# Optimization experiments

Measured on AMD Instinct MI355X. Metric: run time of the kernel, lower is better.

The kernel has to match this reference:

```python
import jax, jax.numpy as jnp
import numpy as np

NH = 12  # attention heads (bert-base)


def _ln(x, s, b, eps=1e-12):
    mu = x.mean(-1, keepdims=True)
    var = ((x - mu) ** 2).mean(-1, keepdims=True)
    return (x - mu) / jnp.sqrt(var + eps) * s + b


def _forward(input_ids, token_type_ids, attention_mask, word_emb, pos_emb, type_emb,
             emb_ln_s, emb_ln_b, memory, q_w, q_b, k_w, k_b, v_w, v_b, o_w, o_b,
             ln1_s, ln1_b, f_w1, f_b1, f_w2, f_b2, ln2_s, ln2_b,
             key_w1, key_b1, key_w2, key_b2, val_w1, val_b1, val_w2, val_b2):
    B, S = input_ids.shape
    M, H = memory.shape
    T = S + M
    m = attention_mask.astype(jnp.int32)          # [B,S] 0/1
    L = m.sum(-1)                                 # [B] number of real tokens
    tok_emb = word_emb[input_ids]                 # [B,S,H]
    # stable argsort puts mask==1 positions first (in original order), then mask==0
    order = jnp.argsort(1 - m, axis=-1)           # [B,S]
    p = jnp.arange(T)[None, :]                    # [1,T]
    Lb = L[:, None]
    # output layout per sample: [real tokens (L), memory (M), pad tokens (S-L)]
    src_p = jnp.clip(jnp.where(p < Lb, p, p - M), 0, S - 1)
    src_idx = jnp.take_along_axis(order, src_p, axis=1)                  # [B,T]
    gathered = jnp.take_along_axis(tok_emb, src_idx[..., None], axis=1)  # [B,T,H]
    is_mem = (p >= Lb) & (p < Lb + M)
    mem_idx = jnp.clip(p - Lb, 0, M - 1)
    emb = jnp.where(is_mem[..., None], memory[mem_idx], gathered)        # spliced embeds
    att = (p < Lb + M).astype(emb.dtype)                                 # [B,T]
    tt = jnp.where(p < Lb, jnp.take_along_axis(token_type_ids.astype(jnp.int32), src_idx, axis=1), 1)
    # --- BERT encoder on inputs_embeds ---
    x = _ln(emb + pos_emb[None, :T] + type_emb[tt], emb_ln_s, emb_ln_b)
    bias = ((1.0 - att) * -10000.0)[:, None, None, :]                    # [B,1,1,T]
    dh = H // NH
    for l in range(q_w.shape[0]):
        q = (x @ q_w[l] + q_b[l]).reshape(B, T, NH, dh)
        k = (x @ k_w[l] + k_b[l]).reshape(B, T, NH, dh)
        v = (x @ v_w[l] + v_b[l]).reshape(B, T, NH, dh)
        s = jnp.einsum('bqhd,bkhd->bhqk', q, k) / jnp.sqrt(jnp.asarray(dh, x.dtype)) + bias
        a = jax.nn.softmax(s, axis=-1)
        ctx = jnp.einsum('bhqk,bkhd->bqhd', a, v).reshape(B, T, H)
        x = _ln(x + ctx @ o_w[l] + o_b[l], ln1_s[l], ln1_b[l])
        h = jax.nn.gelu(x @ f_w1[l] + f_b1[l], approximate=False)
        x = _ln(x + h @ f_w2[l] + f_b2[l], ln2_s[l], ln2_b[l])
    # --- gated key/value softmax pooling (get_rep_no_vae) ---
    value = jnp.tanh(jax.nn.relu(x @ val_w1 + val_b1) @ val_w2 + val_b2)       # [B,T,E]
    weight = jax.nn.sigmoid(jax.nn.relu(x @ key_w1 + key_b1) @ key_w2 + key_b2)  # [B,T,E]
    pool_mask = jnp.where(tt == 1, -jnp.inf, 0.0).astype(x.dtype)[..., None]   # [B,T,1]
    fw = jax.nn.softmax(weight + pool_mask, axis=-2)  # softmax over token dim
    return jax.nn.relu((fw * value).sum(-2))          # [B,E]


def setup_inputs() -> dict:
    key = jax.random.key(0)
    ks = jax.random.split(key, 20)
    B, S, M, H, E, V, NL, FF = 8, 512, 64, 768, 512, 30522, 2, 3072
    def rn(k, shape, s=0.02):
        return jax.random.normal(k, shape, jnp.float32) * s
    return {
        'input_ids': jax.random.randint(ks[0], (B, S), 0, V),
        'token_type_ids': jnp.zeros((B, S), jnp.int32),
        'attention_mask': jax.random.randint(ks[1], (B, S), 0, 2),
        'word_emb': rn(ks[2], (V, H)),
        'pos_emb': rn(ks[3], (S + M, H)),
        'type_emb': rn(ks[4], (2, H)),
        'emb_ln_s': jnp.ones((H,), jnp.float32), 'emb_ln_b': jnp.zeros((H,), jnp.float32),
        'memory': rn(ks[5], (M, H), 1.0),
        'q_w': rn(ks[6], (NL, H, H)), 'q_b': jnp.zeros((NL, H), jnp.float32),
        'k_w': rn(ks[7], (NL, H, H)), 'k_b': jnp.zeros((NL, H), jnp.float32),
        'v_w': rn(ks[8], (NL, H, H)), 'v_b': jnp.zeros((NL, H), jnp.float32),
        'o_w': rn(ks[9], (NL, H, H)), 'o_b': jnp.zeros((NL, H), jnp.float32),
        'ln1_s': jnp.ones((NL, H), jnp.float32), 'ln1_b': jnp.zeros((NL, H), jnp.float32),
        'f_w1': rn(ks[10], (NL, H, FF)), 'f_b1': jnp.zeros((NL, FF), jnp.float32),
        'f_w2': rn(ks[11], (NL, FF, H)), 'f_b2': jnp.zeros((NL, H), jnp.float32),
        'ln2_s': jnp.ones((NL, H), jnp.float32), 'ln2_b': jnp.zeros((NL, H), jnp.float32),
        'key_w1': rn(ks[12], (H, 2 * H)), 'key_b1': jnp.zeros((2 * H,), jnp.float32),
        'key_w2': rn(ks[13], (2 * H, E)), 'key_b2': jnp.zeros((E,), jnp.float32),
        'val_w1': rn(ks[14], (H, 2 * E)), 'val_b1': jnp.zeros((2 * E,), jnp.float32),
        'val_w2': rn(ks[15], (2 * E, E)), 'val_b2': jnp.zeros((E,), jnp.float32),
    }


def reference(input_ids, token_type_ids, attention_mask, word_emb, pos_emb, type_emb,
              emb_ln_s, emb_ln_b, memory, q_w, q_b, k_w, k_b, v_w, v_b, o_w, o_b,
              ln1_s, ln1_b, f_w1, f_b1, f_w2, f_b2, ln2_s, ln2_b,
              key_w1, key_b1, key_w2, key_b2, val_w1, val_b1, val_w2, val_b2):
    return _forward(input_ids, token_type_ids, attention_mask, word_emb, pos_emb, type_emb,
                    emb_ln_s, emb_ln_b, memory, q_w, q_b, k_w, k_b, v_w, v_b, o_w, o_b,
                    ln1_s, ln1_b, f_w1, f_b1, f_w2, f_b2, ln2_s, ln2_b,
                    key_w1, key_b1, key_w2, key_b2, val_w1, val_b1, val_w2, val_b2)
```

## Files before the change

kernel.cpp:

```cpp
#include <hip/hip_runtime.h>
#include <hip/hip_bf16.h>

#define B 8
#define S 512
#define MM 64
#define T 576
#define H 768
#define NH 12
#define DH 64
#define FF 3072
#define E 512
#define NL 2

typedef __attribute__((ext_vector_type(8))) short bf16x8;
typedef __attribute__((ext_vector_type(4))) float f32x4;

__device__ inline unsigned short bf16_rne(float f) {
    unsigned u = __builtin_bit_cast(unsigned, f);
    unsigned r = u + 0x7FFFu + ((u >> 16) & 1u);
    return (unsigned short)(r >> 16);
}

__device__ inline f32x4 mfma16(bf16x8 a, bf16x8 b, f32x4 c) {
    return __builtin_amdgcn_mfma_f32_16x16x32_bf16(a, b, c, 0, 0, 0);
}

__device__ inline void load_lds16(const void* g, void* l) {
    __builtin_amdgcn_global_load_lds((const __attribute__((address_space(1))) void*)g,
                                     (__attribute__((address_space(3))) void*)l, 16, 0, 0);
}

__global__ void embed_kernel(const int* __restrict__ ids, const int* __restrict__ toktype,
                             const int* __restrict__ ord, const int* __restrict__ Larr,
                             int* __restrict__ boff, int* __restrict__ rowb,
                             const float* __restrict__ word_emb, const float* __restrict__ pos_emb,
                             const float* __restrict__ type_emb, const float* __restrict__ memory,
                             const float* __restrict__ lns, const float* __restrict__ lnb,
                             float* __restrict__ x, unsigned short* __restrict__ xb,
                             int* __restrict__ ttarr) {
    int t = blockIdx.x;
    int b = blockIdx.y;
    int pre[B + 1];
    {
        int acc = 0;
        #pragma unroll
        for (int b2 = 0; b2 < B; ++b2) { pre[b2] = acc; acc += Larr[b2] + MM; }
        pre[B] = acc;
    }
    int Lb = Larr[b];
    int tid = threadIdx.x;
    if (t == 0 && b == 0) {
        if (tid <= B) boff[tid] = pre[tid];
        for (int r = tid; r < B * T; r += 256) {
            int bb = 0;
            #pragma unroll
            for (int b2 = 1; b2 < B; ++b2) bb += (r >= pre[b2]) ? 1 : 0;
            rowb[r] = bb;
        }
    }
    if (t >= Lb + MM) return;
    int row = pre[b] + t;
    int tt;
    const float* src;
    if (t < Lb) {
        int sp = ord[b * S + t];
        tt = toktype[b * S + sp];
        src = &word_emb[(size_t)ids[b * S + sp] * H];
    } else {
        tt = 1;
        src = &memory[(size_t)(t - Lb) * H];
    }
    __shared__ float rowv[H];
    __shared__ float r1[256], r2[256];
    float lsum = 0.f, lsq = 0.f;
    for (int hh = tid; hh < H; hh += 256) {
        float v = src[hh] + pos_emb[(size_t)t * H + hh] + type_emb[(size_t)tt * H + hh];
        rowv[hh] = v;
        lsum += v;
        lsq += v * v;
    }
    r1[tid] = lsum; r2[tid] = lsq;
    __syncthreads();
    for (int s = 128; s > 0; s >>= 1) {
        if (tid < s) { r1[tid] += r1[tid + s]; r2[tid] += r2[tid + s]; }
        __syncthreads();
    }
    float mu = r1[0] / H;
    float var = r2[0] / H - mu * mu;
    float inv = rsqrtf(var + 1e-12f);
    for (int hh = tid; hh < H; hh += 256) {
        float v = (rowv[hh] - mu) * inv * lns[hh] + lnb[hh];
        x[(size_t)row * H + hh] = v;
        xb[(size_t)row * H + hh] = bf16_rne(v);
    }
    if (tid == 0) ttarr[row] = tt;
}

#define ACT_NONE 0
#define ACT_RELU 1
#define ACT_GELU 2
#define ACT_SIGMOID 3
#define ACT_TANH 4

template <int ACT>
__device__ inline float apply_act(float v) {
    if constexpr (ACT == ACT_RELU) return fmaxf(v, 0.f);
    else if constexpr (ACT == ACT_GELU) {
        float y = v * 0.70710678118654752f;
        float a = fabsf(y);
        float t = 1.f / (1.f + 0.3275911f * a);
        float poly = t * (0.254829592f + t * (-0.284496736f + t * (1.421413741f +
                     t * (-1.453152027f + t * 1.061405429f))));
        float e = poly * exp2f(-a * a * 1.4426950408889634f);
        float erfv = 1.f - e;
        erfv = (y < 0.f) ? -erfv : erfv;
        return 0.5f * v * (1.f + erfv);
    }
    else if constexpr (ACT == ACT_SIGMOID) return 1.f / (1.f + expf(-v));
    else if constexpr (ACT == ACT_TANH) return tanhf(v);
    else return v;
}

#define NT_TILES 17024
struct TDesc { const float* src; unsigned dstoff; int Kd; int Nd; int tile0; };
struct TTab { TDesc d[16]; int n; };

__global__ __launch_bounds__(256) void transpose_all(TTab tab, unsigned short* __restrict__ dstbase,
                                                     const int* __restrict__ mask,
                                                     int* __restrict__ ord, int* __restrict__ Larr) {
    int tile = blockIdx.x;
    int tid = threadIdx.x;
    if (tile >= NT_TILES) {
        int b = tile - NT_TILES;
        __shared__ int ps[S];
        int m0 = (mask[b * S + tid] != 0) ? 1 : 0;
        int m1 = (mask[b * S + tid + 256] != 0) ? 1 : 0;
        ps[tid] = m0; ps[tid + 256] = m1;
        __syncthreads();
        for (int off2 = 1; off2 < S; off2 <<= 1) {
            int a0 = (tid >= off2) ? ps[tid - off2] : 0;
            int a1 = (tid + 256 >= off2) ? ps[tid + 256 - off2] : 0;
            __syncthreads();
            ps[tid] += a0; ps[tid + 256] += a1;
            __syncthreads();
        }
        int L = ps[S - 1];
        int r0 = m0 ? (ps[tid] - 1) : (L + (tid - ps[tid]));
        int r1 = m1 ? (ps[tid + 256] - 1) : (L + (tid + 256 - ps[tid + 256]));
        ord[b * S + r0] = tid;
        ord[b * S + r1] = tid + 256;
        if (tid == 0) Larr[b] = L;
        return;
    }
    int mi = 0;
    #pragma unroll
    for (int i = 1; i < 16; ++i)
        if (i < tab.n && tab.d[i].tile0 <= tile) mi = i;
    TDesc d = tab.d[mi];
    int rel = tile - d.tile0;
    int tilesK = d.Kd >> 5;
    int kt = rel % tilesK, nt = rel / tilesK;
    __shared__ float ts[32][33];
    int k0 = kt * 32, n0 = nt * 32;
    int tx = tid & 31, ty = tid >> 5;
    #pragma unroll
    for (int r = 0; r < 4; ++r) {
        int kk = ty + r * 8;
        ts[kk][tx] = d.src[(size_t)(k0 + kk) * d.Nd + n0 + tx];
    }
    __syncthreads();
    unsigned short* Wt = dstbase + d.dstoff;
    #pragma unroll
    for (int r = 0; r < 4; ++r) {
        int nn = ty + r * 8;
        Wt[(size_t)(n0 + nn) * d.Kd + k0 + tx] = bf16_rne(ts[tx][nn]);
    }
}

#define EPI_F32   0
#define EPI_BF16  1
#define EPI_QKV   2
#define EPI_SPLIT2 3

template <int ACT, int EPI, int NSPLIT>
__global__ __launch_bounds__(256) void mfma_gemm(
    const unsigned short* __restrict__ A, const unsigned short* __restrict__ Bt,
    const float* __restrict__ b0, const float* __restrict__ b1, const float* __restrict__ b2,
    int sp1, int sp2,
    float* __restrict__ Cf, float* __restrict__ Cf2,
    float* __restrict__ Cf3, float* __restrict__ Cf4,
    unsigned short* __restrict__ Cb, unsigned short* __restrict__ Cb2,
    unsigned short* __restrict__ Vt, int n2w,
    const int* __restrict__ boffs, const int* __restrict__ rowb,
    int Mdim, int Ndim, int Kdim) {
    __shared__ unsigned short As[3][128 * 32];
    __shared__ unsigned short Bs[3][128 * 32];

    const int bn = blockIdx.x * 128, bm = blockIdx.y * 128;

    const int Mtot = boffs[B];
    if (bm >= Mtot) return;

    const int z = (NSPLIT > 1) ? blockIdx.z : 0;
    const int Klocal = Kdim / NSPLIT;
    const int koff = z * Klocal;

    const int tid = threadIdx.x;
    const int w = tid >> 6, lane = tid & 63;
    const int lr = lane & 15, g = lane >> 4;
    const int wr = w >> 1, wc = w & 1;
    f32x4 acc[4][4] = {};

    const int srow = w * 32 + (lane >> 2);
    const int kc = (((lane & 3) ^ ((lane >> 4) & 3)) * 8);
    const unsigned short* ga0 = A + (size_t)(bm + srow) * Kdim + kc;
    const unsigned short* ga1 = A + (size_t)(bm + srow + 16) * Kdim + kc;
    const unsigned short* gb0 = Bt + (size_t)(bn + srow) * Kdim + kc;
    const unsigned short* gb1 = Bt + (size_t)(bn + srow + 16) * Kdim + kc;
    const int d0 = (w * 32) * 32, d1 = (w * 32 + 16) * 32;

    const int sw = ((g ^ ((lr >> 2) & 3)) & 3) * 8;

    auto stage = [&](int pp, int k0) {
        load_lds16(ga0 + k0, &As[pp][d0]);
        load_lds16(ga1 + k0, &As[pp][d1]);
        load_lds16(gb0 + k0, &Bs[pp][d0]);
        load_lds16(gb1 + k0, &Bs[pp][d1]);
    };
    auto compute = [&](int pp) {
        bf16x8 af[4], bfr[4];
        #pragma unroll
        for (int i = 0; i < 4; ++i)
            af[i] = *(const bf16x8*)&As[pp][(wr * 64 + i * 16 + lr) * 32 + sw];
        #pragma unroll
        for (int j = 0; j < 4; ++j)
            bfr[j] = *(const bf16x8*)&Bs[pp][(wc * 64 + j * 16 + lr) * 32 + sw];
        __builtin_amdgcn_s_setprio(1);
        #pragma unroll
        for (int i = 0; i < 4; ++i)
            #pragma unroll
            for (int j = 0; j < 4; ++j)
                acc[i][j] = mfma16(af[i], bfr[j], acc[i][j]);
        __builtin_amdgcn_s_setprio(0);
    };

    const int nk = Klocal >> 5;
    stage(0, koff);
    int p = 0;
    for (int s = 0; s < nk; ++s) {
        if (s + 1 < nk) {
            int pn = p + 1; if (pn == 3) pn = 0;
            stage(pn, koff + (s + 1) * 32);
            asm volatile("s_waitcnt vmcnt(4)" ::: "memory");
        } else {
            asm volatile("s_waitcnt vmcnt(0)" ::: "memory");
        }
        __builtin_amdgcn_s_barrier();
        __builtin_amdgcn_sched_barrier(0);
        compute(p);
        __builtin_amdgcn_sched_barrier(0);
        p = (p == 2) ? 0 : p + 1;
    }

    float* Cdst = (z == 0) ? Cf : (z == 1) ? Cf2 : (z == 2) ? Cf3 : Cf4;
    #pragma unroll
    for (int i = 0; i < 4; ++i) {
        const int row0 = bm + wr * 64 + i * 16 + 4 * g;
        #pragma unroll
        for (int j = 0; j < 4; ++j) {
            const int col = bn + wc * 64 + j * 16 + lr;
            float bv = (NSPLIT > 1 && z != 0) ? 0.f
                     : ((col < sp1) ? b0[col] : (col < sp2 ? b1[col - sp1] : b2[col - sp2]));
            float vv[4];
            #pragma unroll
            for (int r = 0; r < 4; ++r) vv[r] = apply_act<ACT>(acc[i][j][r] + bv);
            if constexpr (EPI == EPI_F32) {
                #pragma unroll
                for (int r = 0; r < 4; ++r) Cdst[(size_t)(row0 + r) * Ndim + col] = vv[r];
            } else if constexpr (EPI == EPI_BF16) {
                #pragma unroll
                for (int r = 0; r < 4; ++r) Cb[(size_t)(row0 + r) * Ndim + col] = bf16_rne(vv[r]);
            } else if constexpr (EPI == EPI_QKV) {
                if (col < 1536) {
                    #pragma unroll
                    for (int r = 0; r < 4; ++r) Cb[(size_t)(row0 + r) * 1536 + col] = bf16_rne(vv[r]);
                } else {
                    int c2 = col - 1536;
                    int hh2 = c2 >> 6, dd = c2 & 63;
                    int bb = rowb[row0];
                    if (row0 + 3 < Mtot && rowb[row0 + 3] == bb) {
                        int t0 = row0 - boffs[bb];
                        unsigned lo = (unsigned)bf16_rne(vv[0]) | ((unsigned)bf16_rne(vv[1]) << 16);
                        unsigned hi = (unsigned)bf16_rne(vv[2]) | ((unsigned)bf16_rne(vv[3]) << 16);
                        size_t idxv = (((size_t)bb * NH + hh2) * DH + dd) * T + t0;
                        *(uint2*)&Vt[idxv] = make_uint2(lo, hi);
                    } else {
                        #pragma unroll
                        for (int r = 0; r < 4; ++r) {
                            int rr = row0 + r;
                            if (rr < Mtot) {
                                int b2 = rowb[rr];
                                int t2 = rr - boffs[b2];
                                Vt[(((size_t)b2 * NH + hh2) * DH + dd) * T + t2] = bf16_rne(vv[r]);
                            }
                        }
                    }
                }
            } else {
                if (col < sp1) {
                    #pragma unroll
                    for (int r = 0; r < 4; ++r) Cb[(size_t)(row0 + r) * sp1 + col] = bf16_rne(vv[r]);
                } else {
                    #pragma unroll
                    for (int r = 0; r < 4; ++r)
                        Cb2[(size_t)(row0 + r) * n2w + (col - sp1)] = bf16_rne(vv[r]);
                }
            }
        }
    }
}

__global__ __launch_bounds__(256) void head2_gemm(
    const unsigned short* __restrict__ Ak, const unsigned short* __restrict__ Btk,
    const float* __restrict__ biask,
    const unsigned short* __restrict__ Av, const unsigned short* __restrict__ Btv,
    const float* __restrict__ biasv,
    float* __restrict__ P0, float* __restrict__ P1, float* __restrict__ P2, float* __restrict__ P3,
    float* __restrict__ V0, float* __restrict__ V1, float* __restrict__ V2, float* __restrict__ V3,
    const int* __restrict__ boffs) {
    __shared__ unsigned short As[3][128 * 32];
    __shared__ unsigned short Bs[3][128 * 32];

    const int bn = blockIdx.x * 128, bm = blockIdx.y * 128;
    const int Mtot = boffs[B];
    if (bm >= Mtot) return;

    const int z = blockIdx.z;
    const int isval = z >> 2, zk = z & 3;
    const unsigned short* A  = isval ? Av : Ak;
    const unsigned short* Bt = isval ? Btv : Btk;
    const float* bias = isval ? biasv : biask;
    const int Kdim = isval ? 1024 : 1536;
    const int Klocal = Kdim >> 2;
    const int koff = zk * Klocal;
    float* Cdst = isval ? ((zk == 0) ? V0 : (zk == 1) ? V1 : (zk == 2) ? V2 : V3)
                        : ((zk == 0) ? P0 : (zk == 1) ? P1 : (zk == 2) ? P2 : P3);

    const int tid = threadIdx.x;
    const int w = tid >> 6, lane = tid & 63;
    const int lr = lane & 15, g = lane >> 4;
    const int wr = w >> 1, wc = w & 1;
    f32x4 acc[4][4] = {};

    const int srow = w * 32 + (lane >> 2);
    const int kc = (((lane & 3) ^ ((lane >> 4) & 3)) * 8);
    const unsigned short* ga0 = A + (size_t)(bm + srow) * Kdim + kc;
    const unsigned short* ga1 = A + (size_t)(bm + srow + 16) * Kdim + kc;
    const unsigned short* gb0 = Bt + (size_t)(bn + srow) * Kdim + kc;
    const unsigned short* gb1 = Bt + (size_t)(bn + srow + 16) * Kdim + kc;
    const int d0 = (w * 32) * 32, d1 = (w * 32 + 16) * 32;
    const int sw = ((g ^ ((lr >> 2) & 3)) & 3) * 8;

    auto stage = [&](int pp, int k0) {
        load_lds16(ga0 + k0, &As[pp][d0]);
        load_lds16(ga1 + k0, &As[pp][d1]);
        load_lds16(gb0 + k0, &Bs[pp][d0]);
        load_lds16(gb1 + k0, &Bs[pp][d1]);
    };
    auto compute = [&](int pp) {
        bf16x8 af[4], bfr[4];
        #pragma unroll
        for (int i = 0; i < 4; ++i)
            af[i] = *(const bf16x8*)&As[pp][(wr * 64 + i * 16 + lr) * 32 + sw];
        #pragma unroll
        for (int j = 0; j < 4; ++j)
            bfr[j] = *(const bf16x8*)&Bs[pp][(wc * 64 + j * 16 + lr) * 32 + sw];
        __builtin_amdgcn_s_setprio(1);
        #pragma unroll
        for (int i = 0; i < 4; ++i)
            #pragma unroll
            for (int j = 0; j < 4; ++j)
                acc[i][j] = mfma16(af[i], bfr[j], acc[i][j]);
        __builtin_amdgcn_s_setprio(0);
    };

    const int nk = Klocal >> 5;
    stage(0, koff);
    int p = 0;
    for (int s = 0; s < nk; ++s) {
        if (s + 1 < nk) {
            int pn = p + 1; if (pn == 3) pn = 0;
            stage(pn, koff + (s + 1) * 32);
            asm volatile("s_waitcnt vmcnt(4)" ::: "memory");
        } else {
            asm volatile("s_waitcnt vmcnt(0)" ::: "memory");
        }
        __builtin_amdgcn_s_barrier();
        __builtin_amdgcn_sched_barrier(0);
        compute(p);
        __builtin_amdgcn_sched_barrier(0);
        p = (p == 2) ? 0 : p + 1;
    }

    #pragma unroll
    for (int i = 0; i < 4; ++i) {
        const int row0 = bm + wr * 64 + i * 16 + 4 * g;
        #pragma unroll
        for (int j = 0; j < 4; ++j) {
            const int col = bn + wc * 64 + j * 16 + lr;
            float bv = (zk == 0) ? bias[col] : 0.f;
            #pragma unroll
            for (int r = 0; r < 4; ++r)
                Cdst[(size_t)(row0 + r) * E + col] = acc[i][j][r] + bv;
        }
    }
}

#define C2 0.180336880111116670f
#define MB2 14426.950408889634f

__global__ __launch_bounds__(256) void attn_mfma(
    const unsigned short* __restrict__ QK, const unsigned short* __restrict__ Vt,
    const int* __restrict__ Larr, const int* __restrict__ boffs,
    unsigned short* __restrict__ ctxb) {
    const int n = blockIdx.x;
    const int xcd = n & 7, k = n >> 3;
    const int p = xcd * 12 + k / 9, qt = k % 9;
    const int b = p / NH, h = p % NH;
    const int LbMM = Larr[b] + MM;
    if (qt * 64 >= LbMM) return;
    const int w = threadIdx.x >> 6, lane = threadIdx.x & 63;
    const int q0 = qt * 64 + w * 16;
    if (q0 >= LbMM) return;
    const int base = boffs[b];
    const int lr = lane & 15, g = lane >> 4;
    __shared__ unsigned short P[4][16][72];
    const unsigned short* qrow = QK + (size_t)(base + q0 + lr) * 1536 + h * 64;
    bf16x8 qf0 = *(const bf16x8*)(qrow + 8 * g);
    bf16x8 qf1 = *(const bf16x8*)(qrow + 32 + 8 * g);
    f32x4 ctx[4] = {};
    float m_run = -1e30f, l_run = 0.f;
    const size_t vbase = ((size_t)b * NH + h) * DH;
    for (int kt = 0; kt < LbMM; kt += 64) {
        f32x4 sf[4];
        #pragma unroll
        for (int i = 0; i < 4; ++i) {
            const unsigned short* krow =
                QK + (size_t)(base + kt + 16 * i + lr) * 1536 + 768 + h * 64;
            bf16x8 kf0 = *(const bf16x8*)(krow + 8 * g);
            bf16x8 kf1 = *(const bf16x8*)(krow + 32 + 8 * g);
            f32x4 s = {};
            s = mfma16(kf0, qf0, s);
            s = mfma16(kf1, qf1, s);
            sf[i] = s;
        }
        float tmax = -1e30f;
        #pragma unroll
        for (int i = 0; i < 4; ++i)
            #pragma unroll
            for (int r = 0; r < 4; ++r) {
                int key = kt + 16 * i + 4 * g + r;
                float v = sf[i][r] * C2 + (key < LbMM ? 0.f : -MB2);
                sf[i][r] = v;
                tmax = fmaxf(tmax, v);
            }
        tmax = fmaxf(tmax, __shfl_xor(tmax, 16));
        tmax = fmaxf(tmax, __shfl_xor(tmax, 32));
        float m_new = fmaxf(m_run, tmax);
        float scale = exp2f(m_run - m_new);
        m_run = m_new;
        float psum = 0.f;
        #pragma unroll
        for (int i = 0; i < 4; ++i)
            #pragma unroll
            for (int r = 0; r < 4; ++r) {
                float pv = exp2f(sf[i][r] - m_new);
                sf[i][r] = pv;
                psum += pv;
            }
        l_run = l_run * scale + psum;
        float f0 = __shfl(scale, 4 * g + 0);
        float f1 = __shfl(scale, 4 * g + 1);
        float f2 = __shfl(scale, 4 * g + 2);
        float f3 = __shfl(scale, 4 * g + 3);
        #pragma unroll
        for (int j = 0; j < 4; ++j) {
            ctx[j][0] *= f0; ctx[j][1] *= f1; ctx[j][2] *= f2; ctx[j][3] *= f3;
        }
        #pragma unroll
        for (int i = 0; i < 4; ++i) {
            unsigned lo = (unsigned)bf16_rne(sf[i][0]) | ((unsigned)bf16_rne(sf[i][1]) << 16);
            unsigned hi = (unsigned)bf16_rne(sf[i][2]) | ((unsigned)bf16_rne(sf[i][3]) << 16);
            *(unsigned*)&P[w][lr][16 * i + 4 * g] = lo;
            *(unsigned*)&P[w][lr][16 * i + 4 * g + 2] = hi;
        }
        asm volatile("s_waitcnt lgkmcnt(0)" ::: "memory");
        __builtin_amdgcn_sched_barrier(0);
        #pragma unroll
        for (int s2 = 0; s2 < 2; ++s2) {
            bf16x8 pa = *(const bf16x8*)&P[w][lr][32 * s2 + 8 * g];
            #pragma unroll
            for (int j = 0; j < 4; ++j) {
                const unsigned short* vrow =
                    Vt + (vbase + 16 * j + lr) * T + kt + 32 * s2 + 8 * g;
                bf16x8 vf = *(const bf16x8*)vrow;
                ctx[j] = mfma16(pa, vf, ctx[j]);
            }
        }
        asm volatile("s_waitcnt lgkmcnt(0)" ::: "memory");
        __builtin_amdgcn_sched_barrier(0);
    }
    l_run += __shfl_xor(l_run, 16);
    l_run += __shfl_xor(l_run, 32);
    float inv = 1.f / l_run;
    float i0 = __shfl(inv, 4 * g + 0);
    float i1 = __shfl(inv, 4 * g + 1);
    float i2 = __shfl(inv, 4 * g + 2);
    float i3 = __shfl(inv, 4 * g + 3);
    float sc[4] = {i0, i1, i2, i3};
    #pragma unroll
    for (int j = 0; j < 4; ++j)
        #pragma unroll
        for (int r = 0; r < 4; ++r) {
            int rl = q0 + 4 * g + r;
            if (rl < LbMM)
                ctxb[(size_t)(base + rl) * H + h * 64 + 16 * j + lr] =
                    bf16_rne(ctx[j][r] * sc[r]);
        }
}

__global__ void lnres_kernel(float* __restrict__ x, const float* __restrict__ d1,
                             const float* __restrict__ d2, const float* __restrict__ d3,
                             const float* __restrict__ d4,
                             const float* __restrict__ s, const float* __restrict__ bvec,
                             unsigned short* __restrict__ xb, const int* __restrict__ mtotp) {
    int r = blockIdx.x;
    if (r >= mtotp[0]) return;
    int tid = threadIdx.x;
    __shared__ float4 row[H / 4];
    __shared__ float r1[256], r2[256];
    float lsum = 0.f, lsq = 0.f;
    size_t off4 = (size_t)r * (H / 4);
    if (tid < H / 4) {
        float4 a = ((const float4*)x)[off4 + tid];
        float4 p1 = ((const float4*)d1)[off4 + tid];
        float4 p2 = ((const float4*)d2)[off4 + tid];
        float4 p3 = ((const float4*)d3)[off4 + tid];
        float4 p4 = ((const float4*)d4)[off4 + tid];
        float4 v = make_float4(a.x + p1.x + p2.x + p3.x + p4.x,
                               a.y + p1.y + p2.y + p3.y + p4.y,
                               a.z + p1.z + p2.z + p3.z + p4.z,
                               a.w + p1.w + p2.w + p3.w + p4.w);
        row[tid] = v;
        lsum = v.x + v.y + v.z + v.w;
        lsq = v.x * v.x + v.y * v.y + v.z * v.z + v.w * v.w;
    }
    r1[tid] = lsum; r2[tid] = lsq;
    __syncthreads();
    for (int ss = 128; ss > 0; ss >>= 1) {
        if (tid < ss) { r1[tid] += r1[tid + ss]; r2[tid] += r2[tid + ss]; }
        __syncthreads();
    }
    float mu = r1[0] / H;
    float var = r2[0] / H - mu * mu;
    float inv = rsqrtf(var + 1e-12f);
    if (tid < H / 4) {
        float4 v = row[tid];
        const float4 sv = ((const float4*)s)[tid];
        const float4 bv = ((const float4*)bvec)[tid];
        float4 o = make_float4((v.x - mu) * inv * sv.x + bv.x,
                               (v.y - mu) * inv * sv.y + bv.y,
                               (v.z - mu) * inv * sv.z + bv.z,
                               (v.w - mu) * inv * sv.w + bv.w);
        ((float4*)x)[off4 + tid] = o;
        ushort4 ob = make_ushort4(bf16_rne(o.x), bf16_rne(o.y), bf16_rne(o.z), bf16_rne(o.w));
        *(ushort4*)&xb[(size_t)r * H + tid * 4] = ob;
    }
}

__global__ __launch_bounds__(256) void pool_kernel(
    const float* __restrict__ w0, const float* __restrict__ w1,
    const float* __restrict__ w2, const float* __restrict__ w3,
    const float* __restrict__ v0, const float* __restrict__ v1,
    const float* __restrict__ v2, const float* __restrict__ v3,
    const int* __restrict__ ttarr, const int* __restrict__ boffs,
    float* __restrict__ out) {
    int b = blockIdx.x;
    int le = threadIdx.x & 31;
    int e = blockIdx.y * 32 + le;
    int tg = threadIdx.x >> 5;
    int base = boffs[b];
    int nrow = boffs[b + 1] - base;
    __shared__ int ttl[T];
    __shared__ float red[8][33];
    for (int t = threadIdx.x; t < nrow; t += 256) ttl[t] = ttarr[base + t];
    __syncthreads();
    float mx = -1e30f;
    for (int t = tg; t < nrow; t += 8) {
        if (ttl[t] == 1) continue;
        size_t idx = (size_t)(base + t) * E + e;
        float w = 1.f / (1.f + expf(-(w0[idx] + w1[idx] + w2[idx] + w3[idx])));
        mx = fmaxf(mx, w);
    }
    red[tg][le] = mx;
    __syncthreads();
    #pragma unroll
    for (int i = 0; i < 8; ++i) mx = fmaxf(mx, red[i][le]);
    float den = 0.f, num = 0.f;
    for (int t = tg; t < nrow; t += 8) {
        if (ttl[t] == 1) continue;
        size_t idx = (size_t)(base + t) * E + e;
        float w = 1.f / (1.f + expf(-(w0[idx] + w1[idx] + w2[idx] + w3[idx])));
        float vval = tanhf(v0[idx] + v1[idx] + v2[idx] + v3[idx]);
        float ew = expf(w - mx);
        den += ew;
        num = fmaf(ew, vval, num);
    }
    __syncthreads();
    red[tg][le] = den;
    __syncthreads();
    float dtot = 0.f;
    #pragma unroll
    for (int i = 0; i < 8; ++i) dtot += red[i][le];
    __syncthreads();
    red[tg][le] = num;
    __syncthreads();
    float ntot = 0.f;
    #pragma unroll
    for (int i = 0; i < 8; ++i) ntot += red[i][le];
    if (tg == 0) out[(size_t)b * E + e] = fmaxf(ntot / dtot, 0.f);
}

extern "C" void kernel_launch(void* const* d_in, const int* in_sizes, int n_in,
                              void* d_out, int out_size, void* d_ws, size_t ws_size,
                              hipStream_t stream) {
    const int*   input_ids  = (const int*)d_in[0];
    const int*   token_type = (const int*)d_in[1];
    const int*   attn_mask  = (const int*)d_in[2];
    const float* word_emb   = (const float*)d_in[3];
    const float* pos_emb    = (const float*)d_in[4];
    const float* type_emb   = (const float*)d_in[5];
    const float* emb_ln_s   = (const float*)d_in[6];
    const float* emb_ln_b   = (const float*)d_in[7];
    const float* memory     = (const float*)d_in[8];
    const float* q_w  = (const float*)d_in[9];
    const float* q_b  = (const float*)d_in[10];
    const float* k_w  = (const float*)d_in[11];
    const float* k_b  = (const float*)d_in[12];
    const float* v_w  = (const float*)d_in[13];
    const float* v_b  = (const float*)d_in[14];
    const float* o_w  = (const float*)d_in[15];
    const float* o_b  = (const float*)d_in[16];
    const float* ln1_s = (const float*)d_in[17];
    const float* ln1_b = (const float*)d_in[18];
    const float* f_w1  = (const float*)d_in[19];
    const float* f_b1  = (const float*)d_in[20];
    const float* f_w2  = (const float*)d_in[21];
    const float* f_b2  = (const float*)d_in[22];
    const float* ln2_s = (const float*)d_in[23];
    const float* ln2_b = (const float*)d_in[24];
    const float* key_w1 = (const float*)d_in[25];
    const float* key_b1 = (const float*)d_in[26];
    const float* key_w2 = (const float*)d_in[27];
    const float* key_b2 = (const float*)d_in[28];
    const float* val_w1 = (const float*)d_in[29];
    const float* val_b1 = (const float*)d_in[30];
    const float* val_w2 = (const float*)d_in[31];
    const float* val_b2 = (const float*)d_in[32];
    float* out = (float*)d_out;

    char* ws = (char*)d_ws;
    size_t off = 0;
    auto alloc = [&](size_t bytes) {
        void* p = ws + off;
        off += (bytes + 255) & ~(size_t)255;
        return p;
    };
    const size_t BT  = (size_t)B * T;
    const size_t BTH = BT * H;

    int*   ord   = (int*)alloc((size_t)B * S * 4);
    int*   Larr  = (int*)alloc(64);
    int*   boff  = (int*)alloc((B + 1) * 4);
    int*   rowb  = (int*)alloc(BT * 4);
    int*   ttarr = (int*)alloc(BT * 4);
    float* x     = (float*)alloc(BTH * 4);
    unsigned short* xb   = (unsigned short*)alloc(BTH * 2);
    unsigned short* reg1 = (unsigned short*)alloc(BT * FF * 2);
    float* P0 = (float*)alloc(BTH * 4);
    float* P1 = (float*)alloc(BTH * 4);
    float* P2 = (float*)alloc(BTH * 4);
    float* P3 = (float*)alloc(BTH * 4);
    float* V0 = (float*)alloc(BT * E * 4);
    float* V1 = (float*)alloc(BT * E * 4);
    float* V2 = (float*)alloc(BT * E * 4);
    float* V3 = (float*)alloc(BT * E * 4);
    unsigned short* wt = (unsigned short*)alloc((size_t)17432576 * 2);

    unsigned short* qkb  = reg1;
    unsigned short* Vtb  = reg1 + BT * 1536;
    unsigned short* ctxb = reg1 + BT * 1536 + BTH;
    unsigned short* hb   = reg1;
    unsigned short* key1b = reg1;
    unsigned short* val1b = reg1 + BT * 1536;

    unsigned short* wt_head = wt + (size_t)14155776;
    unsigned short* wt_kv1 = wt_head;
    unsigned short* wt_k2 = wt_head + (size_t)2560 * 768;
    unsigned short* wt_v2 = wt_k2 + (size_t)512 * 1536;

    const int Mrows = (int)BT;
    const size_t HH = (size_t)H * H;
    const int BIG = 1 << 30;
    const int* mtotp = boff + B;

    {
        TTab tab;
        tab.n = 16;
        for (int l = 0; l < NL; ++l) {
            unsigned base = (unsigned)(l * 7077888);
            int t0 = l * 6912;
            tab.d[l * 6 + 0] = { q_w + l * HH,              base,                        H,  H,  t0        };
            tab.d[l * 6 + 1] = { k_w + l * HH,              base + 768u * 768u,          H,  H,  t0 + 576  };
            tab.d[l * 6 + 2] = { v_w + l * HH,              base + 1536u * 768u,         H,  H,  t0 + 1152 };
            tab.d[l * 6 + 3] = { o_w + l * HH,              base + 2304u * 768u,         H,  H,  t0 + 1728 };
            tab.d[l * 6 + 4] = { f_w1 + (size_t)l * H * FF, base + 3072u * 768u,         H,  FF, t0 + 2304 };
            tab.d[l * 6 + 5] = { f_w2 + (size_t)l * FF * H, base + 6144u * 768u,         FF, H,  t0 + 4608 };
        }
        tab.d[12] = { key_w1, 14155776u,                    H,     2 * H, 13824 };
        tab.d[13] = { val_w1, 14155776u + 1536u * 768u,     H,     2 * E, 14976 };
        tab.d[14] = { key_w2, 16121856u,                    2 * H, E,     15744 };
        tab.d[15] = { val_w2, 16908288u,                    2 * E, E,     16512 };
        hipLaunchKernelGGL(transpose_all, dim3(NT_TILES + B), dim3(256), 0, stream,
                           tab, wt, attn_mask, ord, Larr);
    }

    hipLaunchKernelGGL(embed_kernel, dim3(T, B), dim3(256), 0, stream,
                       input_ids, token_type, ord, Larr, boff, rowb,
                       word_emb, pos_emb, type_emb,
                       memory, emb_ln_s, emb_ln_b, x, xb, ttarr);

    for (int l = 0; l < NL; ++l) {
        unsigned short* wt_l   = wt + (size_t)l * 7077888;
        unsigned short* wt_qkv = wt_l;
        unsigned short* wt_o   = wt_l + (size_t)2304 * 768;
        unsigned short* wt_f1  = wt_o + (size_t)768 * 768;
        unsigned short* wt_f2  = wt_f1 + (size_t)3072 * 768;

        mfma_gemm<ACT_NONE, EPI_QKV, 1><<<dim3(18, 36), 256, 0, stream>>>(
            xb, wt_qkv, q_b + (size_t)l * H, k_b + (size_t)l * H, v_b + (size_t)l * H,
            768, 1536, nullptr, nullptr, nullptr, nullptr, qkb, nullptr, Vtb, 0,
            boff, rowb, Mrows, 2304, H);
        hipLaunchKernelGGL(attn_mfma, dim3(864), dim3(256), 0, stream,
                           qkb, Vtb, Larr, boff, ctxb);
        mfma_gemm<ACT_NONE, EPI_F32, 4><<<dim3(6, 36, 4), 256, 0, stream>>>(
            ctxb, wt_o, o_b + (size_t)l * H, nullptr, nullptr, BIG, BIG,
            P0, P1, P2, P3, nullptr, nullptr, nullptr, 0, boff, rowb, Mrows, H, H);
        hipLaunchKernelGGL(lnres_kernel, dim3((int)BT), dim3(256), 0, stream,
                           x, P0, P1, P2, P3, ln1_s + (size_t)l * H, ln1_b + (size_t)l * H,
                           xb, mtotp);
        mfma_gemm<ACT_GELU, EPI_BF16, 1><<<dim3(24, 36), 256, 0, stream>>>(
            xb, wt_f1, f_b1 + (size_t)l * FF, nullptr, nullptr, BIG, BIG,
            nullptr, nullptr, nullptr, nullptr, hb, nullptr, nullptr, 0,
            boff, rowb, Mrows, FF, H);
        mfma_gemm<ACT_NONE, EPI_F32, 4><<<dim3(6, 36, 4), 256, 0, stream>>>(
            hb, wt_f2, f_b2 + (size_t)l * H, nullptr, nullptr, BIG, BIG,
            P0, P1, P2, P3, nullptr, nullptr, nullptr, 0, boff, rowb, Mrows, H, FF);
        hipLaunchKernelGGL(lnres_kernel, dim3((int)BT), dim3(256), 0, stream,
                           x, P0, P1, P2, P3, ln2_s + (size_t)l * H, ln2_b + (size_t)l * H,
                           xb, mtotp);
    }

    mfma_gemm<ACT_RELU, EPI_SPLIT2, 1><<<dim3(20, 36), 256, 0, stream>>>(
        xb, wt_kv1, key_b1, val_b1, nullptr, 1536, BIG,
        nullptr, nullptr, nullptr, nullptr, key1b, val1b, nullptr, 1024,
        boff, rowb, Mrows, 2560, H);
    head2_gemm<<<dim3(4, 36, 8), 256, 0, stream>>>(
        key1b, wt_k2, key_b2, val1b, wt_v2, val_b2,
        P0, P1, P2, P3, V0, V1, V2, V3, boff);
    hipLaunchKernelGGL(pool_kernel, dim3(B, E / 32), dim3(256), 0, stream,
                       P0, P1, P2, P3, V0, V1, V2, V3, ttarr, boff, out);
}
```

Baseline: 451.4 us.

## Fuse residual LayerNorm into split-K GEMM via last-block atomic counter

Removes the standalone residual+LayerNorm kernels after the O-projection and FFN2 GEMMs. Each split-K GEMM block bumps a per-row-tile atomic counter, and the last block to finish that 128-row tile sums the four partials with the residual, applies LayerNorm and writes both the fp32 and bf16 activations. The counters are zeroed by an extra block in the transpose kernel and reset after use. This saves four kernel launches and their global round trips, at the cost of threadfence/atomic synchronisation and a serial LN tail done by one block per row tile.

```diff
diff --git a/kernel.cpp b/kernel.cpp
--- a/kernel.cpp
+++ b/kernel.cpp
@@ -127,9 +127,14 @@
 
 __global__ __launch_bounds__(256) void transpose_all(TTab tab, unsigned short* __restrict__ dstbase,
                                                      const int* __restrict__ mask,
-                                                     int* __restrict__ ord, int* __restrict__ Larr) {
+                                                     int* __restrict__ ord, int* __restrict__ Larr,
+                                                     int* __restrict__ cnt) {
     int tile = blockIdx.x;
     int tid = threadIdx.x;
+    if (tile >= NT_TILES + B) {
+        if (tid < 64) cnt[tid] = 0;
+        return;
+    }
     if (tile >= NT_TILES) {
         int b = tile - NT_TILES;
         __shared__ int ps[S];
@@ -182,7 +187,7 @@
 #define EPI_QKV   2
 #define EPI_SPLIT2 3
 
-template <int ACT, int EPI, int NSPLIT>
+template <int ACT, int EPI, int NSPLIT, bool LNF>
 __global__ __launch_bounds__(256) void mfma_gemm(
     const unsigned short* __restrict__ A, const unsigned short* __restrict__ Bt,
     const float* __restrict__ b0, const float* __restrict__ b1, const float* __restrict__ b2,
@@ -192,6 +197,8 @@
     unsigned short* __restrict__ Cb, unsigned short* __restrict__ Cb2,
     unsigned short* __restrict__ Vt, int n2w,
     const int* __restrict__ boffs, const int* __restrict__ rowb,
+    const float* __restrict__ lnS, const float* __restrict__ lnB,
+    float* __restrict__ xf, unsigned short* __restrict__ xbo, int* __restrict__ cnt,
     int Mdim, int Ndim, int Kdim) {
     __shared__ unsigned short As[3][128 * 32];
     __shared__ unsigned short Bs[3][128 * 32];
@@ -318,6 +325,48 @@
             }
         }
     }
+
+    if constexpr (LNF) {
+        const int nbm = gridDim.x * NSPLIT;
+        __threadfence();
+        __syncthreads();
+        __shared__ int oldsh;
+        if (tid == 0) oldsh = atomicAdd(&cnt[bm >> 7], 1);
+        __syncthreads();
+        if (oldsh == nbm - 1) {
+            __threadfence();
+            const int wv = tid >> 6, ln2 = tid & 63;
+            for (int rr = wv; rr < 128; rr += 4) {
+                int row = bm + rr;
+                if (row >= Mtot) break;
+                float vals[12];
+                float s1 = 0.f, s2 = 0.f;
+                #pragma unroll
+                for (int c2 = 0; c2 < 12; ++c2) {
+                    size_t idx = (size_t)row * H + c2 * 64 + ln2;
+                    float v = xf[idx] + Cf[idx] + Cf2[idx] + Cf3[idx] + Cf4[idx];
+                    vals[c2] = v; s1 += v; s2 += v * v;
+                }
+                #pragma unroll
+                for (int o = 32; o > 0; o >>= 1) {
+                    s1 += __shfl_xor(s1, o);
+                    s2 += __shfl_xor(s2, o);
+                }
+                float mu = s1 / H;
+                float var = s2 / H - mu * mu;
+                float inv = rsqrtf(var + 1e-12f);
+                #pragma unroll
+                for (int c2 = 0; c2 < 12; ++c2) {
+                    int c = c2 * 64 + ln2;
+                    size_t idx = (size_t)row * H + c;
+                    float o2 = (vals[c2] - mu) * inv * lnS[c] + lnB[c];
+                    xf[idx] = o2;
+                    xbo[idx] = bf16_rne(o2);
+                }
+            }
+            if (tid == 0) cnt[bm >> 7] = 0;
+        }
+    }
 }
 
 __global__ __launch_bounds__(256) void head2_gemm(
@@ -527,55 +576,6 @@
                 ctxb[(size_t)(base + rl) * H + h * 64 + 16 * j + lr] =
                     bf16_rne(ctx[j][r] * sc[r]);
         }
-}
-
-__global__ void lnres_kernel(float* __restrict__ x, const float* __restrict__ d1,
-                             const float* __restrict__ d2, const float* __restrict__ d3,
-                             const float* __restrict__ d4,
-                             const float* __restrict__ s, const float* __restrict__ bvec,
-                             unsigned short* __restrict__ xb, const int* __restrict__ mtotp) {
-    int r = blockIdx.x;
-    if (r >= mtotp[0]) return;
-    int tid = threadIdx.x;
-    __shared__ float4 row[H / 4];
-    __shared__ float r1[256], r2[256];
-    float lsum = 0.f, lsq = 0.f;
-    size_t off4 = (size_t)r * (H / 4);
-    if (tid < H / 4) {
-        float4 a = ((const float4*)x)[off4 + tid];
-        float4 p1 = ((const float4*)d1)[off4 + tid];
-        float4 p2 = ((const float4*)d2)[off4 + tid];
-        float4 p3 = ((const float4*)d3)[off4 + tid];
-        float4 p4 = ((const float4*)d4)[off4 + tid];
-        float4 v = make_float4(a.x + p1.x + p2.x + p3.x + p4.x,
-                               a.y + p1.y + p2.y + p3.y + p4.y,
-                               a.z + p1.z + p2.z + p3.z + p4.z,
-                               a.w + p1.w + p2.w + p3.w + p4.w);
-        row[tid] = v;
-        lsum = v.x + v.y + v.z + v.w;
-        lsq = v.x * v.x + v.y * v.y + v.z * v.z + v.w * v.w;
-    }
-    r1[tid] = lsum; r2[tid] = lsq;
-    __syncthreads();
-    for (int ss = 128; ss > 0; ss >>= 1) {
-        if (tid < ss) { r1[tid] += r1[tid + ss]; r2[tid] += r2[tid + ss]; }
-        __syncthreads();
-    }
-    float mu = r1[0] / H;
-    float var = r2[0] / H - mu * mu;
-    float inv = rsqrtf(var + 1e-12f);
-    if (tid < H / 4) {
-        float4 v = row[tid];
-        const float4 sv = ((const float4*)s)[tid];
-        const float4 bv = ((const float4*)bvec)[tid];
-        float4 o = make_float4((v.x - mu) * inv * sv.x + bv.x,
-                               (v.y - mu) * inv * sv.y + bv.y,
-                               (v.z - mu) * inv * sv.z + bv.z,
-                               (v.w - mu) * inv * sv.w + bv.w);
-        ((float4*)x)[off4 + tid] = o;
-        ushort4 ob = make_ushort4(bf16_rne(o.x), bf16_rne(o.y), bf16_rne(o.z), bf16_rne(o.w));
-        *(ushort4*)&xb[(size_t)r * H + tid * 4] = ob;
-    }
 }
 
 __global__ __launch_bounds__(256) void pool_kernel(
@@ -683,6 +683,7 @@
     int*   Larr  = (int*)alloc(64);
     int*   boff  = (int*)alloc((B + 1) * 4);
     int*   rowb  = (int*)alloc(BT * 4);
+    int*   cnt   = (int*)alloc(64 * 4);
     int*   ttarr = (int*)alloc(BT * 4);
     float* x     = (float*)alloc(BTH * 4);
     unsigned short* xb   = (unsigned short*)alloc(BTH * 2);
@@ -712,7 +713,6 @@
     const int Mrows = (int)BT;
     const size_t HH = (size_t)H * H;
     const int BIG = 1 << 30;
-    const int* mtotp = boff + B;
 
     {
         TTab tab;
@@ -731,8 +731,8 @@
         tab.d[13] = { val_w1, 14155776u + 1536u * 768u,     H,     2 * E, 14976 };
         tab.d[14] = { key_w2, 16121856u,                    2 * H, E,     15744 };
         tab.d[15] = { val_w2, 16908288u,                    2 * E, E,     16512 };
-        hipLaunchKernelGGL(transpose_all, dim3(NT_TILES + B), dim3(256), 0, stream,
-                           tab, wt, attn_mask, ord, Larr);
+        hipLaunchKernelGGL(transpose_all, dim3(NT_TILES + B + 1), dim3(256), 0, stream,
+                           tab, wt, attn_mask, ord, Larr, cnt);
     }
 
     hipLaunchKernelGGL(embed_kernel, dim3(T, B), dim3(256), 0, stream,
@@ -747,34 +747,30 @@
         unsigned short* wt_f1  = wt_o + (size_t)768 * 768;
         unsigned short* wt_f2  = wt_f1 + (size_t)3072 * 768;
 
-        mfma_gemm<ACT_NONE, EPI_QKV, 1><<<dim3(18, 36), 256, 0, stream>>>(
+        mfma_gemm<ACT_NONE, EPI_QKV, 1, false><<<dim3(18, 36), 256, 0, stream>>>(
             xb, wt_qkv, q_b + (size_t)l * H, k_b + (size_t)l * H, v_b + (size_t)l * H,
             768, 1536, nullptr, nullptr, nullptr, nullptr, qkb, nullptr, Vtb, 0,
-            boff, rowb, Mrows, 2304, H);
+            boff, rowb, nullptr, nullptr, nullptr, nullptr, nullptr, Mrows, 2304, H);
         hipLaunchKernelGGL(attn_mfma, dim3(864), dim3(256), 0, stream,
                            qkb, Vtb, Larr, boff, ctxb);
-        mfma_gemm<ACT_NONE, EPI_F32, 4><<<dim3(6, 36, 4), 256, 0, stream>>>(
+        mfma_gemm<ACT_NONE, EPI_F32, 4, true><<<dim3(6, 36, 4), 256, 0, stream>>>(
             ctxb, wt_o, o_b + (size_t)l * H, nullptr, nullptr, BIG, BIG,
-            P0, P1, P2, P3, nullptr, nullptr, nullptr, 0, boff, rowb, Mrows, H, H);
-        hipLaunchKernelGGL(lnres_kernel, dim3((int)BT), dim3(256), 0, stream,
-                           x, P0, P1, P2, P3, ln1_s + (size_t)l * H, ln1_b + (size_t)l * H,
-                           xb, mtotp);
-        mfma_gemm<ACT_GELU, EPI_BF16, 1><<<dim3(24, 36), 256, 0, stream>>>(
+            P0, P1, P2, P3, nullptr, nullptr, nullptr, 0, boff, rowb,
+            ln1_s + (size_t)l * H, ln1_b + (size_t)l * H, x, xb, cnt, Mrows, H, H);
+        mfma_gemm<ACT_GELU, EPI_BF16, 1, false><<<dim3(24, 36), 256, 0, stream>>>(
             xb, wt_f1, f_b1 + (size_t)l * FF, nullptr, nullptr, BIG, BIG,
             nullptr, nullptr, nullptr, nullptr, hb, nullptr, nullptr, 0,
-            boff, rowb, Mrows, FF, H);
-        mfma_gemm<ACT_NONE, EPI_F32, 4><<<dim3(6, 36, 4), 256, 0, stream>>>(
+            boff, rowb, nullptr, nullptr, nullptr, nullptr, nullptr, Mrows, FF, H);
+        mfma_gemm<ACT_NONE, EPI_F32, 4, true><<<dim3(6, 36, 4), 256, 0, stream>>>(
             hb, wt_f2, f_b2 + (size_t)l * H, nullptr, nullptr, BIG, BIG,
-            P0, P1, P2, P3, nullptr, nullptr, nullptr, 0, boff, rowb, Mrows, H, FF);
-        hipLaunchKernelGGL(lnres_kernel, dim3((int)BT), dim3(256), 0, stream,
-                           x, P0, P1, P2, P3, ln2_s + (size_t)l * H, ln2_b + (size_t)l * H,
-                           xb, mtotp);
-    }
-
-    mfma_gemm<ACT_RELU, EPI_SPLIT2, 1><<<dim3(20, 36), 256, 0, stream>>>(
+            P0, P1, P2, P3, nullptr, nullptr, nullptr, 0, boff, rowb,
+            ln2_s + (size_t)l * H, ln2_b + (size_t)l * H, x, xb, cnt, Mrows, H, FF);
+    }
+
+    mfma_gemm<ACT_RELU, EPI_SPLIT2, 1, false><<<dim3(20, 36), 256, 0, stream>>>(
         xb, wt_kv1, key_b1, val_b1, nullptr, 1536, BIG,
         nullptr, nullptr, nullptr, nullptr, key1b, val1b, nullptr, 1024,
-        boff, rowb, Mrows, 2560, H);
+        boff, rowb, nullptr, nullptr, nullptr, nullptr, nullptr, Mrows, 2560, H);
     head2_gemm<<<dim3(4, 36, 8), 256, 0, stream>>>(
         key1b, wt_k2, key_b2, val1b, wt_v2, val_b2,
         P0, P1, P2, P3, V0, V1, V2, V3, boff);
```

Result: slower. 979.7 us (+117.0%).
